# Performance work log

Hardware: AMD Instinct MI355X
Metric: run time of the kernel (lower is better)

The kernel has to match this reference:

```python
import jax, jax.numpy as jnp
import numpy as np

N_NODES = 100000
N_EDGES = 1600000
D_FEAT = 48


def setup_inputs() -> dict:
    key = jax.random.key(0)
    k1, k2, k3, k4 = jax.random.split(key, 4)
    rows = jax.random.randint(k1, (N_EDGES,), 0, N_NODES, dtype=jnp.int32)
    cols = jax.random.randint(k2, (N_EDGES,), 0, N_NODES, dtype=jnp.int32)
    # normalized adjacency values (positive, like D^-1/2 A D^-1/2 entries)
    vals = jax.random.uniform(k3, (N_EDGES,), dtype=jnp.float32)
    embeds = jax.random.normal(k4, (N_NODES, D_FEAT), dtype=jnp.float32)
    return {"rows": rows, "cols": cols, "vals": vals, "embeds": embeds}


def reference(rows, cols, vals, embeds):
    # torch.spmm(adj, embeds) with adj in COO form:
    # out[i] = sum_{e : rows[e]==i} vals[e] * embeds[cols[e]]
    msgs = vals[:, None] * embeds[cols]          # [E, D] gather + scale
    out = jax.ops.segment_sum(msgs, rows, num_segments=embeds.shape[0])  # [N, D]
    return out
```

## Files before the change

kernel.cpp:

```cpp
#include <hip/hip_runtime.h>


#define N_NODES 100000
#define D_FEAT 48
#define DQ (D_FEAT / 4)

#define BUCKET_BITS 7
#define BUCKET_NODES 128
#define N_BUCKETS ((N_NODES + BUCKET_NODES - 1) / BUCKET_NODES)
#define CAPB 2432

#define CHUNK 8192
#define P1_THREADS 1024
#define VPT (CHUNK / P1_THREADS / 4)

#define P2_THREADS 512
#define EPT2 ((CAPB + P2_THREADS - 1) / P2_THREADS)
#define NG (P2_THREADS / 12)

#define PH_SHIFT 14
#define N_PH 8
#define NKEY (N_PH * BUCKET_NODES)

#define OVF_CAP 4096
#define EBF_UINT2 (N_NODES * DQ)

__device__ __forceinline__ unsigned short f2bf(float f) {
    unsigned u = __float_as_uint(f);
    return (unsigned short)((u + 0x7FFFu + ((u >> 16) & 1u)) >> 16);
}

__device__ __forceinline__ float4 bf2f4(uint2 h) {
    float4 m;
    m.x = __uint_as_float((h.x & 0xFFFFu) << 16);
    m.y = __uint_as_float(h.x & 0xFFFF0000u);
    m.z = __uint_as_float((h.y & 0xFFFFu) << 16);
    m.w = __uint_as_float(h.y & 0xFFFF0000u);
    return m;
}

__global__ __launch_bounds__(P1_THREADS) void partition_kernel(
        const int* __restrict__ rows, const int* __restrict__ cols,
        const float* __restrict__ vals, int* __restrict__ gcur,
        uint2* __restrict__ tmp, uint4* __restrict__ ovf, int* __restrict__ novf,
        const float* __restrict__ embeds, uint2* __restrict__ ebf,
        int n_edges) {
    __shared__ int counts[N_BUCKETS];
    __shared__ int cursor[N_BUCKETS];
    __shared__ int gpos[N_BUCKETS];

    int t = threadIdx.x;
    int base = blockIdx.x * CHUNK;
    int n = min(CHUNK, n_edges - base);
    int n4 = n >> 2;

    for (int i = t; i < N_BUCKETS; i += P1_THREADS) { counts[i] = 0; cursor[i] = 0; }
    __syncthreads();

    int      b[VPT * 4];
    unsigned key[VPT * 4];
    float    v[VPT * 4];
    const int4*   rows4 = reinterpret_cast<const int4*>(rows + base);
    const int4*   cols4 = reinterpret_cast<const int4*>(cols + base);
    const float4* vals4 = reinterpret_cast<const float4*>(vals + base);
#pragma unroll
    for (int k = 0; k < VPT; ++k) {
        int idx4 = k * P1_THREADS + t;
        bool ok = idx4 < n4;
        int4   r4 = ok ? rows4[idx4] : make_int4(0, 0, 0, 0);
        int4   c4 = ok ? cols4[idx4] : make_int4(0, 0, 0, 0);
        float4 v4 = ok ? vals4[idx4] : make_float4(0.f, 0.f, 0.f, 0.f);
        int rr[4] = {r4.x, r4.y, r4.z, r4.w};
        int cc[4] = {c4.x, c4.y, c4.z, c4.w};
        float vv[4] = {v4.x, v4.y, v4.z, v4.w};
#pragma unroll
        for (int j = 0; j < 4; ++j) {
            int i = k * 4 + j;
            b[i] = -1;
            if (ok) {
                b[i] = rr[j] >> BUCKET_BITS;
                key[i] = ((unsigned)(rr[j] & (BUCKET_NODES - 1)) << 17) | (unsigned)cc[j];
                v[i] = vv[j];
                atomicAdd(&counts[b[i]], 1);
            }
        }
    }

    if (ebf) {
        const float4* e4 = reinterpret_cast<const float4*>(embeds);
        int stride = gridDim.x * P1_THREADS;
        for (int i = blockIdx.x * P1_THREADS + t; i < EBF_UINT2; i += stride) {
            float4 f = e4[i];
            uint2 p;
            p.x = (unsigned)f2bf(f.x) | ((unsigned)f2bf(f.y) << 16);
            p.y = (unsigned)f2bf(f.z) | ((unsigned)f2bf(f.w) << 16);
            ebf[i] = p;
        }
    }
    __syncthreads();

    for (int i = t; i < N_BUCKETS; i += P1_THREADS)
        gpos[i] = (counts[i] > 0) ? atomicAdd(&gcur[i], counts[i]) : 0;
    __syncthreads();

#pragma unroll
    for (int i = 0; i < VPT * 4; ++i) {
        if (b[i] >= 0) {
            int p = atomicAdd(&cursor[b[i]], 1);
            int pos = gpos[b[i]] + p;
            if (pos < CAPB) {
                tmp[(size_t)b[i] * CAPB + pos] = make_uint2(key[i], __float_as_uint(v[i]));
            } else {
                int o = atomicAdd(novf, 1);
                if (o < OVF_CAP) {
                    unsigned rl = key[i] >> 17;
                    ovf[o] = make_uint4((unsigned)b[i] * BUCKET_NODES + rl,
                                        key[i] & 0x1FFFFu, __float_as_uint(v[i]), 0u);
                }
            }
        }
    }
}

#define ACCUM_OVF_TAIL(GATHER_EXPR)                                             \
    {                                                                           \
        int nov = min(*novf, OVF_CAP);                                          \
        if (nov > 0) {                                                          \
            __syncthreads();                                                    \
            int lo = bkt * BUCKET_NODES, hi = lo + BUCKET_NODES;                \
            for (int i = t; i < nov; i += P2_THREADS) {                         \
                uint4 en = ovf[i];                                              \
                int node = (int)en.x;                                           \
                if (node >= lo && node < hi && node < N_NODES) {                \
                    unsigned c = en.y;                                          \
                    float v = __uint_as_float(en.z);                            \
                    for (int qq = 0; qq < DQ; ++qq) {                           \
                        float4 m = GATHER_EXPR;                                 \
                        float* dst = out + (size_t)node * D_FEAT + qq * 4;      \
                        atomicAdd(dst + 0, v * m.x);                            \
                        atomicAdd(dst + 1, v * m.y);                            \
                        atomicAdd(dst + 2, v * m.z);                            \
                        atomicAdd(dst + 3, v * m.w);                            \
                    }                                                           \
                }                                                               \
            }                                                                   \
        }                                                                       \
    }

__global__ __launch_bounds__(P2_THREADS) void accum_bf16_kernel(
        const int* __restrict__ gcur, const uint2* __restrict__ tmp,
        const uint2* __restrict__ ebf, float* __restrict__ out,
        const int* __restrict__ novf, const uint4* __restrict__ ovf) {
    __shared__ uint2 sorted[CAPB];
    __shared__ int cnt2[NKEY];
    __shared__ int cur2[NKEY];
    __shared__ int off2[NKEY + 1];
    __shared__ int phtot[N_PH];

    int t = threadIdx.x;
    int bkt = blockIdx.x;
    const uint2* bucket = tmp + (size_t)bkt * CAPB;
    int cntE = min(gcur[bkt], CAPB);

    for (int i = t; i < NKEY; i += P2_THREADS) cnt2[i] = 0;
    __syncthreads();

    unsigned kcol[EPT2]; unsigned vbits[EPT2]; int ekey[EPT2];
#pragma unroll
    for (int j = 0; j < EPT2; ++j) {
        int idx = t + j * P2_THREADS;
        ekey[j] = -1;
        if (idx < cntE) {
            uint2 pk = bucket[idx];
            int rl = (int)(pk.x >> 17);
            unsigned col = pk.x & 0x1FFFFu;
            ekey[j] = ((int)(col >> PH_SHIFT) << 7) | rl;
            kcol[j] = col;
            vbits[j] = pk.y;
            atomicAdd(&cnt2[ekey[j]], 1);
        }
    }
    __syncthreads();

    {
        int p = t >> 6, lane = t & 63;
        int k0 = p * BUCKET_NODES + 2 * lane;
        int c0 = cnt2[k0], c1 = cnt2[k0 + 1];
        int s = c0 + c1;
#pragma unroll
        for (int d = 1; d < 64; d <<= 1) {
            int y = __shfl_up(s, d, 64);
            if (lane >= d) s += y;
        }
        if (lane == 63) phtot[p] = s;
        __syncthreads();
        if (t == 0) {
            int run = 0;
#pragma unroll
            for (int i = 0; i < N_PH; ++i) { int a = phtot[i]; phtot[i] = run; run += a; }
        }
        __syncthreads();
        int base = phtot[p] + s - (c0 + c1);
        off2[k0] = base;          cur2[k0] = base;
        off2[k0 + 1] = base + c0; cur2[k0 + 1] = base + c0;
        if (t == 0) off2[NKEY] = cntE;
    }
    __syncthreads();

#pragma unroll
    for (int j = 0; j < EPT2; ++j) {
        if (ekey[j] >= 0) {
            int pos = atomicAdd(&cur2[ekey[j]], 1);
            sorted[pos] = make_uint2(kcol[j], vbits[j]);
        }
    }
    __syncthreads();

    int g = t / 12, q = t - g * 12;
    if (g < NG) {
        float4 acc[4];
#pragma unroll
        for (int k = 0; k < 4; ++k) acc[k] = make_float4(0.f, 0.f, 0.f, 0.f);

        for (int p = 0; p < N_PH; ++p) {
#pragma unroll
            for (int k = 0; k < 4; ++k) {
                int rl = g + k * NG;
                if (rl < BUCKET_NODES) {
                    int key = p * BUCKET_NODES + rl;
                    int e = off2[key], e1 = off2[key + 1];
                    for (; e + 1 < e1; e += 2) {
                        uint2 p0 = sorted[e], p1 = sorted[e + 1];
                        uint2 h0 = ebf[p0.x * DQ + q];
                        uint2 h1 = ebf[p1.x * DQ + q];
                        float4 m0 = bf2f4(h0), m1 = bf2f4(h1);
                        float v0 = __uint_as_float(p0.y), v1 = __uint_as_float(p1.y);
                        acc[k].x += v0 * m0.x; acc[k].y += v0 * m0.y;
                        acc[k].z += v0 * m0.z; acc[k].w += v0 * m0.w;
                        acc[k].x += v1 * m1.x; acc[k].y += v1 * m1.y;
                        acc[k].z += v1 * m1.z; acc[k].w += v1 * m1.w;
                    }
                    if (e < e1) {
                        uint2 p0 = sorted[e];
                        float4 m0 = bf2f4(ebf[p0.x * DQ + q]);
                        float v0 = __uint_as_float(p0.y);
                        acc[k].x += v0 * m0.x; acc[k].y += v0 * m0.y;
                        acc[k].z += v0 * m0.z; acc[k].w += v0 * m0.w;
                    }
                }
            }
        }

#pragma unroll
        for (int k = 0; k < 4; ++k) {
            int rl = g + k * NG;
            if (rl < BUCKET_NODES) {
                int node = bkt * BUCKET_NODES + rl;
                if (node < N_NODES)
                    *(reinterpret_cast<float4*>(out + (size_t)node * D_FEAT) + q) = acc[k];
            }
        }
    }
    ACCUM_OVF_TAIL(bf2f4(ebf[c * DQ + qq]))
}

__global__ __launch_bounds__(P2_THREADS) void accum_f32_kernel(
        const int* __restrict__ gcur, const uint2* __restrict__ tmp,
        const float* __restrict__ embeds, float* __restrict__ out,
        const int* __restrict__ novf, const uint4* __restrict__ ovf) {
    __shared__ uint2 sorted[CAPB];
    __shared__ int cnt[BUCKET_NODES];
    __shared__ int cur[BUCKET_NODES];
    __shared__ int roff[BUCKET_NODES + 1];
    __shared__ int ws2[2];
    int t = threadIdx.x;
    int lane = t & 63;
    int bkt = blockIdx.x;
    const uint2* bucket = tmp + (size_t)bkt * CAPB;
    int cntE = min(gcur[bkt], CAPB);
    if (t < BUCKET_NODES) cnt[t] = 0;
    __syncthreads();
    unsigned kcol[EPT2]; unsigned vbits[EPT2]; int erl[EPT2];
#pragma unroll
    for (int j = 0; j < EPT2; ++j) {
        int idx = t + j * P2_THREADS;
        erl[j] = -1;
        if (idx < cntE) {
            uint2 pk = bucket[idx];
            erl[j] = (int)(pk.x >> 17);
            kcol[j] = pk.x & 0x1FFFFu;
            vbits[j] = pk.y;
            atomicAdd(&cnt[erl[j]], 1);
        }
    }
    __syncthreads();
    int x = 0;
    if (t < BUCKET_NODES) {
        x = cnt[t];
#pragma unroll
        for (int d = 1; d < 64; d <<= 1) {
            int y = __shfl_up(x, d, 64);
            if (lane >= d) x += y;
        }
        if (lane == 63) ws2[t >> 6] = x;
    }
    __syncthreads();
    if (t == 0) { int a = ws2[0]; ws2[0] = 0; ws2[1] = a; }
    __syncthreads();
    if (t < BUCKET_NODES) {
        int incl = x + ws2[t >> 6];
        int st = incl - cnt[t];
        roff[t] = st; cur[t] = st;
    }
    if (t == 0) roff[BUCKET_NODES] = cntE;
    __syncthreads();
#pragma unroll
    for (int j = 0; j < EPT2; ++j) {
        if (erl[j] >= 0) {
            int p = atomicAdd(&cur[erl[j]], 1);
            sorted[p] = make_uint2(kcol[j], vbits[j]);
        }
    }
    __syncthreads();
    int g = t / 12;
    int q = t - g * 12;
    if (g < NG) {
        for (int rl = g; rl < BUCKET_NODES; rl += NG) {
            int s = roff[rl], epos = roff[rl + 1];
            float4 a0 = make_float4(0.f, 0.f, 0.f, 0.f);
            int e = s;
            for (; e < epos; ++e) {
                uint2 p0 = sorted[e];
                float4 m0 = *(reinterpret_cast<const float4*>(embeds + p0.x * D_FEAT) + q);
                float v0 = __uint_as_float(p0.y);
                a0.x += v0 * m0.x; a0.y += v0 * m0.y; a0.z += v0 * m0.z; a0.w += v0 * m0.w;
            }
            int node = bkt * BUCKET_NODES + rl;
            if (node < N_NODES)
                *(reinterpret_cast<float4*>(out + (size_t)node * D_FEAT) + q) = a0;
        }
    }
    ACCUM_OVF_TAIL((*(reinterpret_cast<const float4*>(embeds + (size_t)c * D_FEAT) + qq)))
}

extern "C" void kernel_launch(void* const* d_in, const int* in_sizes, int n_in,
                              void* d_out, int out_size, void* d_ws, size_t ws_size,
                              hipStream_t stream) {
    const int*   rows   = (const int*)d_in[0];
    const int*   cols   = (const int*)d_in[1];
    const float* vals   = (const float*)d_in[2];
    const float* embeds = (const float*)d_in[3];
    float*       out    = (float*)d_out;
    int n_edges = in_sizes[0];

    const size_t TMP_OFF = 4096 + 65536;
    const size_t TMP_SZ  = (size_t)N_BUCKETS * CAPB * sizeof(uint2);
    const size_t EBF_OFF = TMP_OFF + TMP_SZ;
    const size_t EBF_SZ  = (size_t)EBF_UINT2 * sizeof(uint2);
    char* ws = (char*)d_ws;
    int*   gcur = (int*)(ws);
    int*   novf = (int*)(ws + 3200);
    uint4* ovf  = (uint4*)(ws + 4096);
    uint2* tmp  = (uint2*)(ws + TMP_OFF);
    uint2* ebf  = (uint2*)(ws + EBF_OFF);

    bool use_bf16 = ws_size >= EBF_OFF + EBF_SZ;

    hipMemsetAsync(ws, 0, 3264, stream);

    int p1_blocks = (n_edges + CHUNK - 1) / CHUNK;
    partition_kernel<<<p1_blocks, P1_THREADS, 0, stream>>>(
        rows, cols, vals, gcur, tmp, ovf, novf,
        embeds, use_bf16 ? ebf : (uint2*)nullptr, n_edges);

    if (use_bf16)
        accum_bf16_kernel<<<N_BUCKETS, P2_THREADS, 0, stream>>>(gcur, tmp, ebf, out, novf, ovf);
    else
        accum_f32_kernel<<<N_BUCKETS, P2_THREADS, 0, stream>>>(gcur, tmp, embeds, out, novf, ovf);
}
```

Baseline: 136.0 us.

## Drop column-phase sub-sorting, use nontemporal loads/stores, shrink partition chunks

The bf16 accumulate kernel no longer sub-sorts each bucket's edges by column phase. It does a single per-row counting sort and processes one row at a time with a 4-way unrolled gather loop. Streaming reads and writes (edge arrays, embeddings, the tmp buffer, the output) now use nontemporal builtins so single-use data is less likely to pollute cache. The partition kernel uses smaller chunks with fewer threads, giving more blocks and fewer edges per block. Dropping the phase ordering gives up any cache locality it provided for the embedding gathers, in exchange for a simpler prefix scan and less shared memory.

```diff
diff --git a/kernel.cpp b/kernel.cpp
--- a/kernel.cpp
+++ b/kernel.cpp
@@ -10,20 +10,20 @@
 #define N_BUCKETS ((N_NODES + BUCKET_NODES - 1) / BUCKET_NODES)
 #define CAPB 2432
 
-#define CHUNK 8192
-#define P1_THREADS 1024
+#define CHUNK 2048
+#define P1_THREADS 512
 #define VPT (CHUNK / P1_THREADS / 4)
 
 #define P2_THREADS 512
 #define EPT2 ((CAPB + P2_THREADS - 1) / P2_THREADS)
 #define NG (P2_THREADS / 12)
 
-#define PH_SHIFT 14
-#define N_PH 8
-#define NKEY (N_PH * BUCKET_NODES)
-
 #define OVF_CAP 4096
 #define EBF_UINT2 (N_NODES * DQ)
+
+typedef int    i32x4 __attribute__((ext_vector_type(4)));
+typedef float  fl32x4 __attribute__((ext_vector_type(4)));
+typedef unsigned long long u64;
 
 __device__ __forceinline__ unsigned short f2bf(float f) {
     unsigned u = __float_as_uint(f);
@@ -60,16 +60,21 @@
     int      b[VPT * 4];
     unsigned key[VPT * 4];
     float    v[VPT * 4];
-    const int4*   rows4 = reinterpret_cast<const int4*>(rows + base);
-    const int4*   cols4 = reinterpret_cast<const int4*>(cols + base);
-    const float4* vals4 = reinterpret_cast<const float4*>(vals + base);
+    const i32x4*  rows4 = reinterpret_cast<const i32x4*>(rows + base);
+    const i32x4*  cols4 = reinterpret_cast<const i32x4*>(cols + base);
+    const fl32x4* vals4 = reinterpret_cast<const fl32x4*>(vals + base);
 #pragma unroll
     for (int k = 0; k < VPT; ++k) {
         int idx4 = k * P1_THREADS + t;
         bool ok = idx4 < n4;
-        int4   r4 = ok ? rows4[idx4] : make_int4(0, 0, 0, 0);
-        int4   c4 = ok ? cols4[idx4] : make_int4(0, 0, 0, 0);
-        float4 v4 = ok ? vals4[idx4] : make_float4(0.f, 0.f, 0.f, 0.f);
+        i32x4  r4 = {0, 0, 0, 0};
+        i32x4  c4 = {0, 0, 0, 0};
+        fl32x4 v4 = {0.f, 0.f, 0.f, 0.f};
+        if (ok) {
+            r4 = __builtin_nontemporal_load(rows4 + idx4);
+            c4 = __builtin_nontemporal_load(cols4 + idx4);
+            v4 = __builtin_nontemporal_load(vals4 + idx4);
+        }
         int rr[4] = {r4.x, r4.y, r4.z, r4.w};
         int cc[4] = {c4.x, c4.y, c4.z, c4.w};
         float vv[4] = {v4.x, v4.y, v4.z, v4.w};
@@ -87,10 +92,10 @@
     }
 
     if (ebf) {
-        const float4* e4 = reinterpret_cast<const float4*>(embeds);
+        const fl32x4* e4 = reinterpret_cast<const fl32x4*>(embeds);
         int stride = gridDim.x * P1_THREADS;
         for (int i = blockIdx.x * P1_THREADS + t; i < EBF_UINT2; i += stride) {
-            float4 f = e4[i];
+            fl32x4 f = __builtin_nontemporal_load(e4 + i);
             uint2 p;
             p.x = (unsigned)f2bf(f.x) | ((unsigned)f2bf(f.y) << 16);
             p.y = (unsigned)f2bf(f.z) | ((unsigned)f2bf(f.w) << 16);
@@ -109,7 +114,9 @@
             int p = atomicAdd(&cursor[b[i]], 1);
             int pos = gpos[b[i]] + p;
             if (pos < CAPB) {
-                tmp[(size_t)b[i] * CAPB + pos] = make_uint2(key[i], __float_as_uint(v[i]));
+                u64 pk8 = (u64)key[i] | ((u64)__float_as_uint(v[i]) << 32);
+                __builtin_nontemporal_store(
+                    pk8, reinterpret_cast<u64*>(tmp) + (size_t)b[i] * CAPB + pos);
             } else {
                 int o = atomicAdd(novf, 1);
                 if (o < OVF_CAP) {
@@ -152,65 +159,62 @@
         const uint2* __restrict__ ebf, float* __restrict__ out,
         const int* __restrict__ novf, const uint4* __restrict__ ovf) {
     __shared__ uint2 sorted[CAPB];
-    __shared__ int cnt2[NKEY];
-    __shared__ int cur2[NKEY];
-    __shared__ int off2[NKEY + 1];
-    __shared__ int phtot[N_PH];
+    __shared__ int cnt[BUCKET_NODES];
+    __shared__ int cur[BUCKET_NODES];
+    __shared__ int roff[BUCKET_NODES + 1];
+    __shared__ int ws2[2];
 
     int t = threadIdx.x;
+    int lane = t & 63;
     int bkt = blockIdx.x;
     const uint2* bucket = tmp + (size_t)bkt * CAPB;
     int cntE = min(gcur[bkt], CAPB);
 
-    for (int i = t; i < NKEY; i += P2_THREADS) cnt2[i] = 0;
-    __syncthreads();
-
-    unsigned kcol[EPT2]; unsigned vbits[EPT2]; int ekey[EPT2];
+    if (t < BUCKET_NODES) cnt[t] = 0;
+    __syncthreads();
+
+    unsigned kcol[EPT2]; unsigned vbits[EPT2]; int erl[EPT2];
 #pragma unroll
     for (int j = 0; j < EPT2; ++j) {
         int idx = t + j * P2_THREADS;
-        ekey[j] = -1;
+        erl[j] = -1;
         if (idx < cntE) {
-            uint2 pk = bucket[idx];
-            int rl = (int)(pk.x >> 17);
-            unsigned col = pk.x & 0x1FFFFu;
-            ekey[j] = ((int)(col >> PH_SHIFT) << 7) | rl;
-            kcol[j] = col;
-            vbits[j] = pk.y;
-            atomicAdd(&cnt2[ekey[j]], 1);
-        }
-    }
-    __syncthreads();
-
-    {
-        int p = t >> 6, lane = t & 63;
-        int k0 = p * BUCKET_NODES + 2 * lane;
-        int c0 = cnt2[k0], c1 = cnt2[k0 + 1];
-        int s = c0 + c1;
+            u64 pk8 = __builtin_nontemporal_load(
+                reinterpret_cast<const u64*>(bucket) + idx);
+            unsigned kx = (unsigned)pk8;
+            erl[j] = (int)(kx >> 17);
+            kcol[j] = kx & 0x1FFFFu;
+            vbits[j] = (unsigned)(pk8 >> 32);
+            atomicAdd(&cnt[erl[j]], 1);
+        }
+    }
+    __syncthreads();
+
+    int x = 0;
+    if (t < BUCKET_NODES) {
+        x = cnt[t];
 #pragma unroll
         for (int d = 1; d < 64; d <<= 1) {
-            int y = __shfl_up(s, d, 64);
-            if (lane >= d) s += y;
-        }
-        if (lane == 63) phtot[p] = s;
-        __syncthreads();
-        if (t == 0) {
-            int run = 0;
-#pragma unroll
-            for (int i = 0; i < N_PH; ++i) { int a = phtot[i]; phtot[i] = run; run += a; }
-        }
-        __syncthreads();
-        int base = phtot[p] + s - (c0 + c1);
-        off2[k0] = base;          cur2[k0] = base;
-        off2[k0 + 1] = base + c0; cur2[k0 + 1] = base + c0;
-        if (t == 0) off2[NKEY] = cntE;
-    }
+            int y = __shfl_up(x, d, 64);
+            if (lane >= d) x += y;
+        }
+        if (lane == 63) ws2[t >> 6] = x;
+    }
+    __syncthreads();
+    if (t == 0) { int a = ws2[0]; ws2[0] = 0; ws2[1] = a; }
+    __syncthreads();
+    if (t < BUCKET_NODES) {
+        int incl = x + ws2[t >> 6];
+        int st = incl - cnt[t];
+        roff[t] = st; cur[t] = st;
+    }
+    if (t == 0) roff[BUCKET_NODES] = cntE;
     __syncthreads();
 
 #pragma unroll
     for (int j = 0; j < EPT2; ++j) {
-        if (ekey[j] >= 0) {
-            int pos = atomicAdd(&cur2[ekey[j]], 1);
+        if (erl[j] >= 0) {
+            int pos = atomicAdd(&cur[erl[j]], 1);
             sorted[pos] = make_uint2(kcol[j], vbits[j]);
         }
     }
@@ -218,46 +222,37 @@
 
     int g = t / 12, q = t - g * 12;
     if (g < NG) {
-        float4 acc[4];
-#pragma unroll
-        for (int k = 0; k < 4; ++k) acc[k] = make_float4(0.f, 0.f, 0.f, 0.f);
-
-        for (int p = 0; p < N_PH; ++p) {
-#pragma unroll
-            for (int k = 0; k < 4; ++k) {
-                int rl = g + k * NG;
-                if (rl < BUCKET_NODES) {
-                    int key = p * BUCKET_NODES + rl;
-                    int e = off2[key], e1 = off2[key + 1];
-                    for (; e + 1 < e1; e += 2) {
-                        uint2 p0 = sorted[e], p1 = sorted[e + 1];
-                        uint2 h0 = ebf[p0.x * DQ + q];
-                        uint2 h1 = ebf[p1.x * DQ + q];
-                        float4 m0 = bf2f4(h0), m1 = bf2f4(h1);
-                        float v0 = __uint_as_float(p0.y), v1 = __uint_as_float(p1.y);
-                        acc[k].x += v0 * m0.x; acc[k].y += v0 * m0.y;
-                        acc[k].z += v0 * m0.z; acc[k].w += v0 * m0.w;
-                        acc[k].x += v1 * m1.x; acc[k].y += v1 * m1.y;
-                        acc[k].z += v1 * m1.z; acc[k].w += v1 * m1.w;
-                    }
-                    if (e < e1) {
-                        uint2 p0 = sorted[e];
-                        float4 m0 = bf2f4(ebf[p0.x * DQ + q]);
-                        float v0 = __uint_as_float(p0.y);
-                        acc[k].x += v0 * m0.x; acc[k].y += v0 * m0.y;
-                        acc[k].z += v0 * m0.z; acc[k].w += v0 * m0.w;
-                    }
-                }
-            }
-        }
-
-#pragma unroll
-        for (int k = 0; k < 4; ++k) {
-            int rl = g + k * NG;
-            if (rl < BUCKET_NODES) {
-                int node = bkt * BUCKET_NODES + rl;
-                if (node < N_NODES)
-                    *(reinterpret_cast<float4*>(out + (size_t)node * D_FEAT) + q) = acc[k];
+        const uint2* ebq = ebf + q;
+        for (int rl = g; rl < BUCKET_NODES; rl += NG) {
+            int e = roff[rl], e1 = roff[rl + 1];
+            float4 a = make_float4(0.f, 0.f, 0.f, 0.f);
+            for (; e + 3 < e1; e += 4) {
+                uint2 p0 = sorted[e],     p1 = sorted[e + 1];
+                uint2 p2 = sorted[e + 2], p3 = sorted[e + 3];
+                uint2 h0 = ebq[p0.x * DQ];
+                uint2 h1 = ebq[p1.x * DQ];
+                uint2 h2 = ebq[p2.x * DQ];
+                uint2 h3 = ebq[p3.x * DQ];
+                float v0 = __uint_as_float(p0.y), v1 = __uint_as_float(p1.y);
+                float v2 = __uint_as_float(p2.y), v3 = __uint_as_float(p3.y);
+                float4 m0 = bf2f4(h0), m1 = bf2f4(h1);
+                float4 m2 = bf2f4(h2), m3 = bf2f4(h3);
+                a.x += v0 * m0.x; a.y += v0 * m0.y; a.z += v0 * m0.z; a.w += v0 * m0.w;
+                a.x += v1 * m1.x; a.y += v1 * m1.y; a.z += v1 * m1.z; a.w += v1 * m1.w;
+                a.x += v2 * m2.x; a.y += v2 * m2.y; a.z += v2 * m2.z; a.w += v2 * m2.w;
+                a.x += v3 * m3.x; a.y += v3 * m3.y; a.z += v3 * m3.z; a.w += v3 * m3.w;
+            }
+            for (; e < e1; ++e) {
+                uint2 p0 = sorted[e];
+                float4 m0 = bf2f4(ebq[p0.x * DQ]);
+                float v0 = __uint_as_float(p0.y);
+                a.x += v0 * m0.x; a.y += v0 * m0.y; a.z += v0 * m0.z; a.w += v0 * m0.w;
+            }
+            int node = bkt * BUCKET_NODES + rl;
+            if (node < N_NODES) {
+                fl32x4 av = {a.x, a.y, a.z, a.w};
+                __builtin_nontemporal_store(
+                    av, reinterpret_cast<fl32x4*>(out + (size_t)node * D_FEAT) + q);
             }
         }
     }
```

Result: slower. 181.4 us (+33.4%).
